# Performance work log

Measured on AMD Instinct MI355X. Metric: run time of the kernel, lower is better.

## Reference

```python
import jax, jax.numpy as jnp
import numpy as np

BS, S, D, H, HS, HSEL, L = 32, 512, 512, 8, 2, 4, 6
DK = D // H  # 64
HD = H - HS  # dynamic heads


def setup_inputs() -> dict:
    key = jax.random.key(0)
    ks = jax.random.split(key, 10)
    w = lambda k, shape: jax.random.normal(k, shape, dtype=jnp.float32) * 0.02
    return {
        'q_embed_data': jax.random.normal(ks[0], (BS, S, D), jnp.float32),
        'qa_embed_data': jax.random.normal(ks[1], (BS, S, D), jnp.float32),
        # stacked per-layer params (torch Linear convention: W[out,in], y = x@W.T+b)
        'Wq': w(ks[2], (L, D, D)), 'bq': jnp.zeros((L, D), jnp.float32),
        'Wv': w(ks[3], (L, D, D)), 'bv': jnp.zeros((L, D), jnp.float32),
        'Wg': w(ks[4], (L, HD, D)),                      # routing gate, no bias
        'Wo': w(ks[5], (L, D, D)), 'bo': jnp.zeros((L, D), jnp.float32),
        'ln1_g': jnp.ones((L, D), jnp.float32), 'ln1_b': jnp.zeros((L, D), jnp.float32),
        'W1': w(ks[6], (L, D, D)), 'b1': jnp.zeros((L, D), jnp.float32),
        'W2': w(ks[7], (L, D, D)), 'b2': jnp.zeros((L, D), jnp.float32),
        'ln2_g': jnp.ones((L, D), jnp.float32), 'ln2_b': jnp.zeros((L, D), jnp.float32),
    }


def _layer_norm(x, g, b):
    m = x.mean(-1, keepdims=True)
    v = ((x - m) ** 2).mean(-1, keepdims=True)
    return (x - m) * jax.lax.rsqrt(v + 1e-5) * g + b


def _moh_attention(xq, xv, Wq, bq, Wv, bv, Wg, Wo, bo, strict):
    bs, s, d = xq.shape
    q = xq @ Wq.T + bq            # kq_same=True: k = q projection
    v = xv @ Wv.T + bv
    qh = q.reshape(bs, s, H, DK).transpose(0, 2, 1, 3)   # [b,h,s,dk]
    vh = v.reshape(bs, s, H, DK).transpose(0, 2, 1, 3)
    scores = jnp.einsum('bhqd,bhkd->bhqk', qh, qh) / jnp.sqrt(jnp.float32(DK))
    # mask==1 -> causal incl. diag; mask==0 -> strictly causal
    allow = jnp.tril(jnp.ones((s, s), bool), k=-1 if strict else 0)
    scores = jnp.where(allow, scores, jnp.float32(-1e9))
    # pad-zero shift: first query row replaced by zeros -> uniform attention
    scores = scores.at[:, :, 0, :].set(0.0)
    # per-token top-k head routing over dynamic heads
    gates = jax.nn.softmax(q.reshape(bs * s, D) @ Wg.T, axis=-1)  # [bs*s, HD]
    _, idx = jax.lax.top_k(gates, HSEL)
    dmask = jnp.zeros_like(gates).at[jnp.arange(bs * s)[:, None], idx].set(1.0)
    dyn = (gates * dmask).reshape(bs, s, HD)
    routing = jnp.concatenate([jnp.ones((bs, s, HS), gates.dtype), dyn], -1).mean(1)  # [b,H]
    attn = jax.nn.softmax(scores, axis=-1)
    ctx = jnp.einsum('bhqk,bhkd->bhqd', attn, vh) * routing[:, :, None, None]
    out = ctx.transpose(0, 2, 1, 3).reshape(bs, s, D) @ Wo.T + bo
    f = dmask.sum(0)
    P = gates.mean(0)
    balance = jnp.sum((f / (f.sum() + 1e-5)) * (P / (P.sum() + 1e-5)))
    return out, balance


def reference(q_embed_data, qa_embed_data, Wq, bq, Wv, bv, Wg, Wo, bo,
              ln1_g, ln1_b, W1, b1, W2, b2, ln2_g, ln2_b):
    def layer(i, xq, xv, strict):
        a, bl = _moh_attention(xq, xv, Wq[i], bq[i], Wv[i], bv[i], Wg[i], Wo[i], bo[i], strict)
        x = _layer_norm(xq + a, ln1_g[i], ln1_b[i])
        ffn = jax.nn.relu(x @ W1[i].T + b1[i]) @ W2[i].T + b2[i]
        return _layer_norm(x + ffn, ln2_g[i], ln2_b[i]), bl

    y = qa_embed_data
    x = q_embed_data
    # blocks_1: self-attention on y, mask=1
    y, _ = layer(0, y, y, False)
    y, _ = layer(1, y, y, False)
    # blocks_2: alternate mask=1 self-attn / mask=0 cross-attn (values=y)
    x, _ = layer(2, x, x, False)
    x, bl = layer(3, x, y, True)
    x, _ = layer(4, x, x, False)
    x, bl = layer(5, x, y, True)
    return (x, bl)
```

## Files before the change

kernel.cpp:

```cpp
#include <hip/hip_runtime.h>
#include <cstdint>

#define BSZ 32
#define SEQ 512
#define DM  512
#define NH  8
#define DK  64
#define HS_ 2
#define HD_ 6
#define NL  6
#define MROWS (BSZ*SEQ)
#define QVLD 1024
#define SCL 0.18033688011112043f

typedef unsigned short bf16_t;
typedef __attribute__((ext_vector_type(4))) float f32x4;
typedef __attribute__((ext_vector_type(8))) short bf16x8;
typedef __attribute__((ext_vector_type(8))) unsigned short u16x8;

#define DEV static __device__ __forceinline__

DEV float bf2f(bf16_t b) {
  unsigned int u = ((unsigned int)b) << 16;
  float f; __builtin_memcpy(&f, &u, 4); return f;
}
DEV bf16_t f2b(float f) {
  unsigned int u; __builtin_memcpy(&u, &f, 4);
  unsigned int r = (u + 0x7fffu + ((u >> 16) & 1u)) >> 16;
  return (bf16_t)r;
}
DEV void unp2(unsigned int w, float& a, float& b) {
  unsigned int ua = w << 16, ub = w & 0xffff0000u;
  __builtin_memcpy(&a, &ua, 4); __builtin_memcpy(&b, &ub, 4);
}
DEV unsigned cvtpk(float lo, float hi) {
  unsigned r;
  asm("v_cvt_pk_bf16_f32 %0, %1, %2" : "=v"(r) : "v"(lo), "v"(hi));
  return r;
}

DEV void gload_lds16(const bf16_t* g, bf16_t* l) {
  __builtin_amdgcn_global_load_lds(
      (const __attribute__((address_space(1))) void*)g,
      (__attribute__((address_space(3))) void*)l, 16, 0, 0);
}

DEV bf16x8 scale_q(bf16x8 v) {
  u16x8 u;
  __builtin_memcpy(&u, &v, 16);
  unsigned w[4];
#pragma unroll
  for (int e = 0; e < 4; ++e)
    w[e] = cvtpk(bf2f(u[2 * e]) * SCL, bf2f(u[2 * e + 1]) * SCL);
  bf16x8 r;
  __builtin_memcpy(&r, w, 16);
  return r;
}

__global__ __launch_bounds__(256) void f2b2_kernel(
    const float* __restrict__ s0, const float* __restrict__ s1,
    bf16_t* __restrict__ d0, bf16_t* __restrict__ d1) {
  const float* s = blockIdx.y ? s1 : s0;
  bf16_t* d = blockIdx.y ? d1 : d0;
  const int i = blockIdx.x * 256 + threadIdx.x;
  float4 v = reinterpret_cast<const float4*>(s)[i];
  ushort4 o;
  o.x = f2b(v.x); o.y = f2b(v.y); o.z = f2b(v.z); o.w = f2b(v.w);
  reinterpret_cast<ushort4*>(d)[i] = o;
}

__global__ __launch_bounds__(256) void f2bw_kernel(
    const float* __restrict__ s0, const float* __restrict__ s1,
    const float* __restrict__ s2, const float* __restrict__ s3,
    const float* __restrict__ s4, bf16_t* __restrict__ dst) {
  const float* srcs[5] = {s0, s1, s2, s3, s4};
  const float* s = srcs[blockIdx.y];
  bf16_t* d = dst + (size_t)blockIdx.y * ((size_t)NL * DM * DM);
  const int i = blockIdx.x * 256 + threadIdx.x;
  float4 v = reinterpret_cast<const float4*>(s)[i];
  ushort4 o;
  o.x = f2b(v.x); o.y = f2b(v.y); o.z = f2b(v.z); o.w = f2b(v.w);
  reinterpret_cast<ushort4*>(d)[i] = o;
}

template <int NB, int NWG, bool RELU>
__global__ __launch_bounds__(512) void gemm8(
    const bf16_t* __restrict__ A0, const bf16_t* __restrict__ A1,
    const bf16_t* __restrict__ W0, const bf16_t* __restrict__ W1,
    const float* __restrict__ b0, const float* __restrict__ b1,
    bf16_t* __restrict__ Yb, int ldy) {
  const int K = 512;
  const int lin = blockIdx.y * NB + blockIdx.x;
  const int cpx = NWG / 8;
  const int swz = (lin & 7) * cpx + (lin >> 3);
  const int bn = swz % NB, bm = swz / NB;
  const int tid = threadIdx.x, wid = tid >> 6, lane = tid & 63;
  const int wr = wid >> 2, wc = wid & 3;
  const int lrow = lane & 15, grp = lane >> 4;
  const int l3 = lane >> 3, c3 = lane & 7;

  __shared__ __align__(16) bf16_t Lds[3][24576];

  const bool hi = (bn * 256) >= 512;
  const bf16_t* Asel = hi ? A1 : A0;
  const bf16_t* Wsel = hi ? (W1 - (size_t)512 * K) : W0;
  const float* bsel = hi ? (b1 - 512) : b0;

  f32x4 acc[4][4];
#pragma unroll
  for (int m = 0; m < 4; ++m)
#pragma unroll
    for (int n = 0; n < 4; ++n) acc[m][n] = f32x4{0.f, 0.f, 0.f, 0.f};

  const char* LB = (const char*)Lds;

  auto stage3 = [&](int kt, int buf, int half) {
#pragma unroll
    for (int cc = 0; cc < 3; ++cc) {
      const int c = wid + (half * 3 + cc) * 8;
      const int colb = ((c3 ^ l3) * 8);
      if (c < 16) {
        gload_lds16(Asel + (size_t)(bm * 128 + c * 8 + l3) * K + kt * 64 + colb,
                    &Lds[buf][c * 512]);
      } else {
        const int cb = c - 16;
        gload_lds16(Wsel + (size_t)(bn * 256 + cb * 8 + l3) * K + kt * 64 + colb,
                    &Lds[buf][8192 + cb * 512]);
      }
    }
  };
  auto rdA = [&](int buf, int rA, int ks) -> bf16x8 {
    const int off = buf * 49152 + rA * 128 + ((ks * 64 + grp * 16) ^ ((rA & 7) << 4));
    return *reinterpret_cast<const bf16x8*>(LB + off);
  };
  auto rdB = [&](int buf, int rB, int ks) -> bf16x8 {
    const int off = buf * 49152 + 16384 + rB * 128 + ((ks * 64 + grp * 16) ^ ((rB & 7) << 4));
    return *reinterpret_cast<const bf16x8*>(LB + off);
  };

  stage3(0, 0, 0); stage3(0, 0, 1);
  stage3(1, 1, 0); stage3(1, 1, 1);
  asm volatile("s_waitcnt vmcnt(6)" ::: "memory");
  __builtin_amdgcn_s_barrier();

  for (int g = 0; g < 8; ++g) {
    const int bufR = g % 3, bufW = (g + 2) % 3;
    const bool st = g < 6;
    bf16x8 bwv[4][2], afv[2][2];
#pragma unroll
    for (int n = 0; n < 4; ++n)
#pragma unroll
      for (int ks = 0; ks < 2; ++ks)
        bwv[n][ks] = rdB(bufR, wc * 64 + n * 16 + lrow, ks);
#pragma unroll
    for (int m = 0; m < 2; ++m)
#pragma unroll
      for (int ks = 0; ks < 2; ++ks)
        afv[m][ks] = rdA(bufR, wr * 64 + m * 16 + lrow, ks);
    if (st) stage3(g + 2, bufW, 0);
    __builtin_amdgcn_s_barrier();
    asm volatile("s_waitcnt lgkmcnt(0)" ::: "memory");
    __builtin_amdgcn_s_setprio(1);
#pragma unroll
    for (int ks = 0; ks < 2; ++ks)
#pragma unroll
      for (int m = 0; m < 2; ++m)
#pragma unroll
        for (int n = 0; n < 4; ++n)
          acc[m][n] = __builtin_amdgcn_mfma_f32_16x16x32_bf16(afv[m][ks], bwv[n][ks], acc[m][n], 0, 0, 0);
    __builtin_amdgcn_s_setprio(0);
    __builtin_amdgcn_s_barrier();
#pragma unroll
    for (int m = 0; m < 2; ++m)
#pragma unroll
      for (int ks = 0; ks < 2; ++ks)
        afv[m][ks] = rdA(bufR, wr * 64 + 32 + m * 16 + lrow, ks);
    if (st) stage3(g + 2, bufW, 1);
    __builtin_amdgcn_s_barrier();
    asm volatile("s_waitcnt lgkmcnt(0)" ::: "memory");
    __builtin_amdgcn_s_setprio(1);
#pragma unroll
    for (int ks = 0; ks < 2; ++ks)
#pragma unroll
      for (int m = 0; m < 2; ++m)
#pragma unroll
        for (int n = 0; n < 4; ++n)
          acc[2 + m][n] = __builtin_amdgcn_mfma_f32_16x16x32_bf16(afv[m][ks], bwv[n][ks], acc[2 + m][n], 0, 0, 0);
    __builtin_amdgcn_s_setprio(0);
    if (g < 6) {
      asm volatile("s_waitcnt vmcnt(6)" ::: "memory");
    } else if (g == 6) {
      asm volatile("s_waitcnt vmcnt(0)" ::: "memory");
    }
    __builtin_amdgcn_s_barrier();
  }

  const int r0 = bm * 128 + wr * 64 + grp * 4;
  const int c0 = bn * 256 + wc * 64 + lrow;
#pragma unroll
  for (int n = 0; n < 4; ++n) {
    const int col = c0 + n * 16;
    const float bc = bsel[col];
#pragma unroll
    for (int qm = 0; qm < 4; ++qm)
#pragma unroll
      for (int j = 0; j < 4; ++j) {
        float v = acc[qm][n][j] + bc;
        if (RELU) v = fmaxf(v, 0.f);
        Yb[(size_t)(r0 + qm * 16 + j) * ldy + col] = f2b(v);
      }
  }
}

template <int OUT>
__global__ __launch_bounds__(512) void gemm_ln(
    const bf16_t* __restrict__ A, const bf16_t* __restrict__ W,
    const float* __restrict__ bias, const bf16_t* __restrict__ Res,
    const float* __restrict__ gam, const float* __restrict__ bet,
    bf16_t* __restrict__ outb, float* __restrict__ outf) {
  const int K = 512;
  const int bm = blockIdx.x;
  const int tid = threadIdx.x, wid = tid >> 6, lane = tid & 63;
  const int lrow = lane & 15, grp = lane >> 4;
  const int l3 = lane >> 3, c3 = lane & 7;

  __shared__ __align__(16) bf16_t Lds[2][36864];
  __shared__ float red_s[64][8], red_q[64][8], stat[64][2];

  f32x4 acc[4][4];
#pragma unroll
  for (int m = 0; m < 4; ++m)
#pragma unroll
    for (int n = 0; n < 4; ++n) acc[m][n] = f32x4{0.f, 0.f, 0.f, 0.f};

  const char* LB = (const char*)Lds;

  auto stage = [&](int kt, int buf) {
#pragma unroll
    for (int k = 0; k < 9; ++k) {
      const int c = wid + k * 8;
      const int colb = (c3 ^ l3) * 8;
      if (c < 8) {
        gload_lds16(A + (size_t)(bm * 64 + c * 8 + l3) * K + kt * 64 + colb,
                    &Lds[buf][c * 512]);
      } else {
        const int cb = c - 8;
        gload_lds16(W + (size_t)(cb * 8 + l3) * K + kt * 64 + colb,
                    &Lds[buf][4096 + cb * 512]);
      }
    }
  };
  auto rdA = [&](int buf, int r, int ks) -> bf16x8 {
    const int off = buf * 73728 + r * 128 + ((ks * 64 + grp * 16) ^ ((r & 7) << 4));
    return *reinterpret_cast<const bf16x8*>(LB + off);
  };
  auto rdW = [&](int buf, int r, int ks) -> bf16x8 {
    const int off = buf * 73728 + 8192 + r * 128 + ((ks * 64 + grp * 16) ^ ((r & 7) << 4));
    return *reinterpret_cast<const bf16x8*>(LB + off);
  };

  stage(0, 0);
  __syncthreads();
  for (int g = 0; g < 8; ++g) {
    const int bufR = g & 1;
    if (g < 7) stage(g + 1, bufR ^ 1);
    bf16x8 af[4][2], wf[4][2];
#pragma unroll
    for (int m = 0; m < 4; ++m)
#pragma unroll
      for (int ks = 0; ks < 2; ++ks)
        af[m][ks] = rdA(bufR, m * 16 + lrow, ks);
#pragma unroll
    for (int n = 0; n < 4; ++n)
#pragma unroll
      for (int ks = 0; ks < 2; ++ks)
        wf[n][ks] = rdW(bufR, wid * 64 + n * 16 + lrow, ks);
    __builtin_amdgcn_s_setprio(1);
#pragma unroll
    for (int ks = 0; ks < 2; ++ks)
#pragma unroll
      for (int m = 0; m < 4; ++m)
#pragma unroll
        for (int n = 0; n < 4; ++n)
          acc[m][n] = __builtin_amdgcn_mfma_f32_16x16x32_bf16(af[m][ks], wf[n][ks], acc[m][n], 0, 0, 0);
    __builtin_amdgcn_s_setprio(0);
    __syncthreads();
  }

  const int cbase = wid * 64;
  float bias_n[4], gam_n[4], bet_n[4];
#pragma unroll
  for (int n = 0; n < 4; ++n) {
    bias_n[n] = bias[cbase + n * 16 + lrow];
    gam_n[n]  = gam[cbase + n * 16 + lrow];
    bet_n[n]  = bet[cbase + n * 16 + lrow];
  }
  const size_t rowg0 = (size_t)bm * 64;
  float ps[4][4], pq[4][4];
#pragma unroll
  for (int m = 0; m < 4; ++m)
#pragma unroll
    for (int j = 0; j < 4; ++j) {
      const int r = m * 16 + grp * 4 + j;
      float s = 0.f, q = 0.f;
#pragma unroll
      for (int n = 0; n < 4; ++n) {
        float z = acc[m][n][j] + bias_n[n] +
                  bf2f(Res[(rowg0 + r) * DM + cbase + n * 16 + lrow]);
        acc[m][n][j] = z;
        s += z; q += z * z;
      }
      ps[m][j] = s; pq[m][j] = q;
    }
#pragma unroll
  for (int m = 0; m < 4; ++m)
#pragma unroll
    for (int j = 0; j < 4; ++j)
#pragma unroll
      for (int off = 1; off <= 8; off <<= 1) {
        ps[m][j] += __shfl_xor(ps[m][j], off);
        pq[m][j] += __shfl_xor(pq[m][j], off);
      }
  if (lrow == 0) {
#pragma unroll
    for (int m = 0; m < 4; ++m)
#pragma unroll
      for (int j = 0; j < 4; ++j) {
        const int r = m * 16 + grp * 4 + j;
        red_s[r][wid] = ps[m][j];
        red_q[r][wid] = pq[m][j];
      }
  }
  __syncthreads();
  if (tid < 64) {
    float s = 0.f, q = 0.f;
#pragma unroll
    for (int w = 0; w < 8; ++w) { s += red_s[tid][w]; q += red_q[tid][w]; }
    const float mean = s * (1.f / 512.f);
    const float var = q * (1.f / 512.f) - mean * mean;
    stat[tid][0] = mean;
    stat[tid][1] = rsqrtf(var + 1e-5f);
  }
  __syncthreads();
#pragma unroll
  for (int m = 0; m < 4; ++m)
#pragma unroll
    for (int j = 0; j < 4; ++j) {
      const int r = m * 16 + grp * 4 + j;
      const float mean = stat[r][0], rstd = stat[r][1];
#pragma unroll
      for (int n = 0; n < 4; ++n) {
        const float o = (acc[m][n][j] - mean) * rstd * gam_n[n] + bet_n[n];
        const size_t off = (rowg0 + r) * DM + cbase + n * 16 + lrow;
        if (OUT == 0) outb[off] = f2b(o);
        else outf[off] = o;
      }
    }
}

__global__ __launch_bounds__(256) void gates_kernel(
    const bf16_t* __restrict__ qv, const float* __restrict__ Wg,
    float* __restrict__ rdyn, float* __restrict__ fP) {
  __shared__ float wg_s[HD_ * DM];
  __shared__ float blk[4][18];
  const int tid = threadIdx.x, wid = tid >> 6, lane = tid & 63;
  for (int i = tid; i < HD_ * DM / 4; i += 256)
    reinterpret_cast<float4*>(wg_s)[i] = reinterpret_cast<const float4*>(Wg)[i];
  __syncthreads();
  const int bb = blockIdx.x >> 4;
  const int t0 = (blockIdx.x & 15) * 32 + wid * 8;
  float fs[6] = {0, 0, 0, 0, 0, 0}, ps[6] = {0, 0, 0, 0, 0, 0}, rs[6] = {0, 0, 0, 0, 0, 0};
  for (int it = 0; it < 8; ++it) {
    const int tok = bb * SEQ + t0 + it;
    uint4 u = reinterpret_cast<const uint4*>(qv + (size_t)tok * QVLD)[lane];
    float x[8];
    unp2(u.x, x[0], x[1]); unp2(u.y, x[2], x[3]);
    unp2(u.z, x[4], x[5]); unp2(u.w, x[6], x[7]);
    float g[6];
#pragma unroll
    for (int j = 0; j < 6; ++j) {
      float p = 0.f;
#pragma unroll
      for (int e = 0; e < 8; ++e) p = fmaf(x[e], wg_s[j * DM + lane * 8 + e], p);
#pragma unroll
      for (int off = 32; off; off >>= 1) p += __shfl_xor(p, off);
      g[j] = p;
    }
    float mx = g[0];
#pragma unroll
    for (int j = 1; j < 6; ++j) mx = fmaxf(mx, g[j]);
    float se = 0.f;
#pragma unroll
    for (int j = 0; j < 6; ++j) { g[j] = __expf(g[j] - mx); se += g[j]; }
    float inv = 1.f / se;
#pragma unroll
    for (int j = 0; j < 6; ++j) g[j] *= inv;
    int d1 = 0;
#pragma unroll
    for (int j = 1; j < 6; ++j)
      if (g[j] < g[d1] || (g[j] == g[d1] && j > d1)) d1 = j;
    int d2 = (d1 == 0) ? 1 : 0;
#pragma unroll
    for (int j = 0; j < 6; ++j) {
      if (j == d1) continue;
      if (g[j] < g[d2] || (g[j] == g[d2] && j > d2)) d2 = j;
    }
#pragma unroll
    for (int j = 0; j < 6; ++j) {
      const bool drop = (j == d1) || (j == d2);
      fs[j] += drop ? 0.f : 1.f;
      ps[j] += g[j];
      rs[j] += drop ? 0.f : g[j];
    }
  }
  if (lane == 0) {
#pragma unroll
    for (int j = 0; j < 6; ++j) {
      blk[wid][j] = fs[j]; blk[wid][6 + j] = ps[j]; blk[wid][12 + j] = rs[j];
    }
  }
  __syncthreads();
  if (tid < 18) {
    float s = blk[0][tid] + blk[1][tid] + blk[2][tid] + blk[3][tid];
    if (tid < 12) atomicAdd(&fP[tid], s);
    else atomicAdd(&rdyn[bb * 6 + (tid - 12)], s * (1.f / 512.f));
  }
}

__global__ __launch_bounds__(256, 2) void fattn_kernel(
    const bf16_t* __restrict__ qv, const float* __restrict__ rdyn,
    bf16_t* __restrict__ ctx, int strict) {
  const int bh = blockIdx.x, qt = blockIdx.y;
  const int b = bh >> 3, h = bh & 7;
  const int tid = threadIdx.x, wid = tid >> 6, lane = tid & 63;
  const int c0 = lane & 15, grp = lane >> 4;
  const int l3 = lane >> 3, c3 = lane & 7;
  const int kidx = lane & 31, dhalf = lane >> 5;

  __shared__ __align__(16) bf16_t Ks[64 * 64];
  __shared__ __align__(16) bf16_t Vt[64 * 72];
  __shared__ __align__(16) bf16_t Ps[4][32 * 64];
  __shared__ float csum[64];

  const bf16_t* qp = qv;
  const bf16_t* vp = qv + 512;
  const float factor = (h < HS_) ? 1.f : rdyn[b * 6 + (h - HS_)];

  const int qbase = qt * 128 + wid * 32;

  bf16x8 qf[2][2];
#pragma unroll
  for (int nt = 0; nt < 2; ++nt)
#pragma unroll
    for (int ks = 0; ks < 2; ++ks)
      qf[nt][ks] = scale_q(*reinterpret_cast<const bf16x8*>(
          qp + ((size_t)(b * SEQ + qbase + nt * 16 + c0)) * QVLD + h * DK + ks * 32 + grp * 8));

  f32x4 acc[2][4];
#pragma unroll
  for (int m = 0; m < 2; ++m)
#pragma unroll
    for (int d = 0; d < 4; ++d) acc[m][d] = f32x4{0.f, 0.f, 0.f, 0.f};
  float mreg[2] = {-3e38f, -3e38f};
  float lreg[2] = {0.f, 0.f};
  float cs[8] = {0, 0, 0, 0, 0, 0, 0, 0};

  const int lastk = (qbase + 31 - strict) >> 6;
  const int ktmax = 2 * qt + 1;

  for (int kt = 0; kt <= ktmax; ++kt) {
#pragma unroll
    for (int i = 0; i < 2; ++i) {
      int row = i * 32 + wid * 8 + l3;
      int blk = c3 ^ l3;
      gload_lds16(qp + ((size_t)(b * SEQ + kt * 64 + row)) * QVLD + h * DK + blk * 8,
                  Ks + (i * 32 + wid * 8) * 64);
    }
#pragma unroll
    for (int j = 0; j < 2; ++j) {
      const int d0 = (wid * 2 + j) * 8 + dhalf * 4;
      const bf16_t* src = vp + ((size_t)(b * SEQ + kt * 64 + 2 * kidx)) * QVLD + h * DK + d0;
      ushort4 lo = *reinterpret_cast<const ushort4*>(src);
      ushort4 hv = *reinterpret_cast<const ushort4*>(src + QVLD);
      *reinterpret_cast<unsigned*>(&Vt[(d0 + 0) * 72 + 2 * kidx]) = (unsigned)lo.x | ((unsigned)hv.x << 16);
      *reinterpret_cast<unsigned*>(&Vt[(d0 + 1) * 72 + 2 * kidx]) = (unsigned)lo.y | ((unsigned)hv.y << 16);
      *reinterpret_cast<unsigned*>(&Vt[(d0 + 2) * 72 + 2 * kidx]) = (unsigned)lo.z | ((unsigned)hv.z << 16);
      *reinterpret_cast<unsigned*>(&Vt[(d0 + 3) * 72 + 2 * kidx]) = (unsigned)lo.w | ((unsigned)hv.w << 16);
      if (qt == 3) {
        cs[j * 4 + 0] += bf2f(lo.x) + bf2f(hv.x);
        cs[j * 4 + 1] += bf2f(lo.y) + bf2f(hv.y);
        cs[j * 4 + 2] += bf2f(lo.z) + bf2f(hv.z);
        cs[j * 4 + 3] += bf2f(lo.w) + bf2f(hv.w);
      }
    }
    __syncthreads();

    if (kt <= lastk) {
      const char* KsB = (const char*)Ks;
      bf16x8 kf[4][2];
#pragma unroll
      for (int mt = 0; mt < 4; ++mt)
#pragma unroll
        for (int ks = 0; ks < 2; ++ks)
          kf[mt][ks] = *reinterpret_cast<const bf16x8*>(
              KsB + (mt * 16 + c0) * 128 + 16 * ((4 * ks + grp) ^ (c0 & 7)));
      f32x4 s[4][2];
#pragma unroll
      for (int mt = 0; mt < 4; ++mt)
#pragma unroll
        for (int nt = 0; nt < 2; ++nt) s[mt][nt] = f32x4{0.f, 0.f, 0.f, 0.f};
      __builtin_amdgcn_s_setprio(1);
#pragma unroll
      for (int mt = 0; mt < 4; ++mt)
#pragma unroll
        for (int nt = 0; nt < 2; ++nt)
#pragma unroll
          for (int ks = 0; ks < 2; ++ks)
            s[mt][nt] = __builtin_amdgcn_mfma_f32_16x16x32_bf16(
                kf[mt][ks], qf[nt][ks], s[mt][nt], 0, 0, 0);
      __builtin_amdgcn_s_setprio(0);

      const bool masked = (kt == lastk);
      if (masked) {
#pragma unroll
        for (int nt = 0; nt < 2; ++nt) {
          const int q = qbase + nt * 16 + c0;
#pragma unroll
          for (int mt = 0; mt < 4; ++mt)
#pragma unroll
            for (int j = 0; j < 4; ++j) {
              int k = kt * 64 + mt * 16 + grp * 4 + j;
              if (k + strict > q) s[mt][nt][j] = -1e30f;
            }
        }
      }
      float mx[2];
#pragma unroll
      for (int nt = 0; nt < 2; ++nt) {
        float a = fmaxf(s[0][nt][0], s[0][nt][1]);
        a = fmaxf(fmaxf(a, s[0][nt][2]), s[0][nt][3]);
        float bm_ = fmaxf(s[1][nt][0], s[1][nt][1]);
        bm_ = fmaxf(fmaxf(bm_, s[1][nt][2]), s[1][nt][3]);
        float c = fmaxf(s[2][nt][0], s[2][nt][1]);
        c = fmaxf(fmaxf(c, s[2][nt][2]), s[2][nt][3]);
        float d = fmaxf(s[3][nt][0], s[3][nt][1]);
        d = fmaxf(fmaxf(d, s[3][nt][2]), s[3][nt][3]);
        float m_ = fmaxf(fmaxf(a, bm_), fmaxf(c, d));
        m_ = fmaxf(m_, __shfl_xor(m_, 16));
        m_ = fmaxf(m_, __shfl_xor(m_, 32));
        mx[nt] = m_;
      }
      const bool defer = __all((mx[0] - mreg[0] <= 8.f) && (mx[1] - mreg[1] <= 8.f));
      float sc[2];
#pragma unroll
      for (int nt = 0; nt < 2; ++nt) {
        const float mnew = defer ? mreg[nt] : fmaxf(mreg[nt], mx[nt]);
        float ts = 0.f;
#pragma unroll
        for (int mt = 0; mt < 4; ++mt)
#pragma unroll
          for (int j = 0; j < 4; ++j) {
            float pp = exp2f(s[mt][nt][j] - mnew);
            s[mt][nt][j] = pp; ts += pp;
          }
        ts += __shfl_xor(ts, 16);
        ts += __shfl_xor(ts, 32);
        if (defer) {
          lreg[nt] += ts;
        } else {
          sc[nt] = exp2f(mreg[nt] - mnew);
          lreg[nt] = lreg[nt] * sc[nt] + ts;
          mreg[nt] = mnew;
        }
      }
      char* PsB = (char*)(&Ps[wid][0]);
#pragma unroll
      for (int nt = 0; nt < 2; ++nt)
#pragma unroll
        for (int mt = 0; mt < 4; ++mt) {
          uint2 w;
          w.x = cvtpk(s[mt][nt][0], s[mt][nt][1]);
          w.y = cvtpk(s[mt][nt][2], s[mt][nt][3]);
          int row = nt * 16 + c0;
          int off = (row * 128 + mt * 32 + grp * 8) ^ ((c0 & 7) << 4);
          *reinterpret_cast<uint2*>(PsB + off) = w;
        }
      if (!defer) {
#pragma unroll
        for (int mtq = 0; mtq < 2; ++mtq) {
          f32x4 sv;
#pragma unroll
          for (int j = 0; j < 4; ++j) sv[j] = __shfl(sc[mtq], grp * 4 + j);
#pragma unroll
          for (int dt = 0; dt < 4; ++dt) acc[mtq][dt] *= sv;
        }
      }
      bf16x8 pf[2][2], vf2[4][2];
#pragma unroll
      for (int mtq = 0; mtq < 2; ++mtq)
#pragma unroll
        for (int ks = 0; ks < 2; ++ks)
          pf[mtq][ks] = *reinterpret_cast<const bf16x8*>(
              PsB + (mtq * 16 + c0) * 128 + 16 * ((4 * ks + grp) ^ (c0 & 7)));
#pragma unroll
      for (int dt = 0; dt < 4; ++dt)
#pragma unroll
        for (int ks = 0; ks < 2; ++ks)
          vf2[dt][ks] = *reinterpret_cast<const bf16x8*>(
              (const char*)Vt + (dt * 16 + c0) * 144 + ks * 64 + grp * 16);
      __builtin_amdgcn_s_setprio(1);
#pragma unroll
      for (int mtq = 0; mtq < 2; ++mtq)
#pragma unroll
        for (int dt = 0; dt < 4; ++dt)
#pragma unroll
          for (int ks = 0; ks < 2; ++ks)
            acc[mtq][dt] = __builtin_amdgcn_mfma_f32_16x16x32_bf16(
                pf[mtq][ks], vf2[dt][ks], acc[mtq][dt], 0, 0, 0);
      __builtin_amdgcn_s_setprio(0);
    }
    __syncthreads();
  }

  if (qt == 3) {
#pragma unroll
    for (int e = 0; e < 8; ++e)
#pragma unroll
      for (int off = 1; off <= 16; off <<= 1) cs[e] += __shfl_xor(cs[e], off);
    if ((lane & 31) == 0) {
#pragma unroll
      for (int e = 0; e < 8; ++e)
        csum[(wid * 2 + (e >> 2)) * 8 + dhalf * 4 + (e & 3)] = cs[e];
    }
    __syncthreads();
    if (tid < 64)
      ctx[((size_t)(b * SEQ)) * DM + h * DK + tid] = f2b(csum[tid] * (1.f / 512.f) * factor);
  }

#pragma unroll
  for (int mtq = 0; mtq < 2; ++mtq) {
    const float inv = factor / lreg[mtq];
    f32x4 iv;
#pragma unroll
    for (int j = 0; j < 4; ++j) iv[j] = __shfl(inv, grp * 4 + j);
#pragma unroll
    for (int j = 0; j < 4; ++j) {
      const int q = qbase + mtq * 16 + grp * 4 + j;
      if (q == 0) continue;
#pragma unroll
      for (int dt = 0; dt < 4; ++dt)
        ctx[((size_t)(b * SEQ + q)) * DM + h * DK + dt * 16 + c0] =
            f2b(acc[mtq][dt][j] * iv[j]);
    }
  }
}

__global__ void balance_kernel(const float* __restrict__ fP, float* __restrict__ out) {
  if (threadIdx.x == 0 && blockIdx.x == 0) {
    float fs = 0.f, pssum = 0.f, P[6];
    for (int j = 0; j < 6; ++j) {
      fs += fP[j];
      P[j] = fP[6 + j] * (1.f / (float)MROWS);
      pssum += P[j];
    }
    float bal = 0.f;
    for (int j = 0; j < 6; ++j)
      bal += (fP[j] / (fs + 1e-5f)) * (P[j] / (pssum + 1e-5f));
    out[0] = bal;
  }
}

extern "C" void kernel_launch(void* const* d_in, const int* in_sizes, int n_in,
                              void* d_out, int out_size, void* d_ws, size_t ws_size,
                              hipStream_t stream) {
  (void)in_sizes; (void)n_in; (void)out_size; (void)ws_size;
  const float* q_embed  = (const float*)d_in[0];
  const float* qa_embed = (const float*)d_in[1];
  const float* Wq  = (const float*)d_in[2];
  const float* bq  = (const float*)d_in[3];
  const float* Wv  = (const float*)d_in[4];
  const float* bv  = (const float*)d_in[5];
  const float* Wg  = (const float*)d_in[6];
  const float* Wo  = (const float*)d_in[7];
  const float* bo  = (const float*)d_in[8];
  const float* ln1g = (const float*)d_in[9];
  const float* ln1b = (const float*)d_in[10];
  const float* W1  = (const float*)d_in[11];
  const float* b1  = (const float*)d_in[12];
  const float* W2  = (const float*)d_in[13];
  const float* b2  = (const float*)d_in[14];
  const float* ln2g = (const float*)d_in[15];
  const float* ln2b = (const float*)d_in[16];

  char* p = (char*)d_ws;
  auto alloc = [&](size_t bytes) -> char* {
    char* r = p; p += (bytes + 255) & ~(size_t)255; return r;
  };
  const size_t WDE = (size_t)NL * DM * DM;
  const size_t AE  = (size_t)MROWS * DM;
  bf16_t* wall_b = (bf16_t*)alloc(5 * WDE * 2);
  bf16_t* wq_b = wall_b;
  bf16_t* wv_b = wall_b + WDE;
  bf16_t* wo_b = wall_b + 2 * WDE;
  bf16_t* w1_b = wall_b + 3 * WDE;
  bf16_t* w2_b = wall_b + 4 * WDE;
  bf16_t* y_b   = (bf16_t*)alloc(AE * 2);
  bf16_t* x_b   = (bf16_t*)alloc(AE * 2);
  bf16_t* qv_b  = (bf16_t*)alloc((size_t)MROWS * QVLD * 2);
  bf16_t* ctx_b = (bf16_t*)alloc(AE * 2);
  bf16_t* x1_b  = (bf16_t*)alloc(AE * 2);
  bf16_t* ffn1_b = (bf16_t*)alloc(AE * 2);
  float* stats = (float*)alloc(NL * (12 + BSZ * 6) * 4);
  float* fPbase = stats;
  float* rdynbase = stats + NL * 12;

  hipMemsetAsync(stats, 0, NL * (12 + BSZ * 6) * 4, stream);

  f2bw_kernel<<<dim3((unsigned)(WDE / 4 / 256), 5), 256, 0, stream>>>(
      Wq, Wv, Wo, W1, W2, wall_b);
  f2b2_kernel<<<dim3((unsigned)(AE / 4 / 256), 2), 256, 0, stream>>>(
      qa_embed, q_embed, y_b, x_b);

  const size_t DD = (size_t)DM * DM;
  dim3 gqv(4, 128), gn5(2, 128), gfa(256, 4), gln(256);
  float* outx = (float*)d_out;

  auto layer = [&](int i, bf16_t* resb, const bf16_t* xvb, int strict, bool last) {
    float* fP = fPbase + i * 12;
    float* rdyn = rdynbase + i * (BSZ * 6);
    gemm8<4, 512, false><<<gqv, 512, 0, stream>>>(
        resb, xvb, wq_b + i * DD, wv_b + i * DD, bq + i * DM, bv + i * DM, qv_b, QVLD);
    gates_kernel<<<MROWS / 32, 256, 0, stream>>>(qv_b, Wg + (size_t)i * HD_ * DM, rdyn, fP);
    fattn_kernel<<<gfa, 256, 0, stream>>>(qv_b, rdyn, ctx_b, strict);
    gemm_ln<0><<<gln, 512, 0, stream>>>(
        ctx_b, wo_b + i * DD, bo + i * DM, resb, ln1g + i * DM, ln1b + i * DM,
        x1_b, nullptr);
    gemm8<2, 256, true><<<gn5, 512, 0, stream>>>(
        x1_b, x1_b, w1_b + i * DD, w1_b + i * DD, b1 + i * DM, b1 + i * DM, ffn1_b, DM);
    if (last)
      gemm_ln<1><<<gln, 512, 0, stream>>>(
          ffn1_b, w2_b + i * DD, b2 + i * DM, x1_b, ln2g + i * DM, ln2b + i * DM,
          nullptr, outx);
    else
      gemm_ln<0><<<gln, 512, 0, stream>>>(
          ffn1_b, w2_b + i * DD, b2 + i * DM, x1_b, ln2g + i * DM, ln2b + i * DM,
          resb, nullptr);
  };

  layer(0, y_b, y_b, 0, false);
  layer(1, y_b, y_b, 0, false);
  layer(2, x_b, x_b, 0, false);
  layer(3, x_b, y_b, 1, false);
  layer(4, x_b, x_b, 0, false);
  layer(5, x_b, y_b, 1, true);
  balance_kernel<<<1, 64, 0, stream>>>(fPbase + 5 * 12, outx + (size_t)MROWS * DM);
}
```

Baseline: 887.7 us.

## Restructure gemm_ln into 4-wave, triple-buffered K=32 pipeline with wider per-wave tiles

The fused GEMM+LayerNorm kernel now runs 256 threads (4 waves) instead of 8. Each wave computes 128 output columns, and K is stepped in 32-wide slices through a 3-deep LDS ring buffer. Explicit vmcnt waits and raw barriers replace __syncthreads, so loads can stay two stages ahead of the MFMAs. The cost is fewer waves per block and more accumulator registers, which may lower occupancy. The new unswizzled LDS layout may also cause bank conflicts.

```diff
diff --git a/kernel.cpp b/kernel.cpp
--- a/kernel.cpp
+++ b/kernel.cpp
@@ -213,7 +213,7 @@
 }
 
 template <int OUT>
-__global__ __launch_bounds__(512) void gemm_ln(
+__global__ __launch_bounds__(256) void gemm_ln(
     const bf16_t* __restrict__ A, const bf16_t* __restrict__ W,
     const float* __restrict__ bias, const bf16_t* __restrict__ Res,
     const float* __restrict__ gam, const float* __restrict__ bet,
@@ -222,75 +222,74 @@
   const int bm = blockIdx.x;
   const int tid = threadIdx.x, wid = tid >> 6, lane = tid & 63;
   const int lrow = lane & 15, grp = lane >> 4;
-  const int l3 = lane >> 3, c3 = lane & 7;
-
-  __shared__ __align__(16) bf16_t Lds[2][36864];
-  __shared__ float red_s[64][8], red_q[64][8], stat[64][2];
-
-  f32x4 acc[4][4];
+  const int prow = lane >> 2, pcol = (lane & 3) * 8;
+
+  __shared__ __align__(16) bf16_t Lds[3][18432];
+  __shared__ float red_s[64][4], red_q[64][4], stat[64][2];
+
+  f32x4 acc[4][8];
 #pragma unroll
   for (int m = 0; m < 4; ++m)
 #pragma unroll
-    for (int n = 0; n < 4; ++n) acc[m][n] = f32x4{0.f, 0.f, 0.f, 0.f};
+    for (int n = 0; n < 8; ++n) acc[m][n] = f32x4{0.f, 0.f, 0.f, 0.f};
 
   const char* LB = (const char*)Lds;
 
   auto stage = [&](int kt, int buf) {
 #pragma unroll
     for (int k = 0; k < 9; ++k) {
-      const int c = wid + k * 8;
-      const int colb = (c3 ^ l3) * 8;
-      if (c < 8) {
-        gload_lds16(A + (size_t)(bm * 64 + c * 8 + l3) * K + kt * 64 + colb,
+      const int c = wid * 9 + k;
+      if (c < 4) {
+        gload_lds16(A + (size_t)(bm * 64 + c * 16 + prow) * K + kt * 32 + pcol,
                     &Lds[buf][c * 512]);
       } else {
-        const int cb = c - 8;
-        gload_lds16(W + (size_t)(cb * 8 + l3) * K + kt * 64 + colb,
-                    &Lds[buf][4096 + cb * 512]);
+        const int w = c - 4;
+        gload_lds16(W + (size_t)(w * 16 + prow) * K + kt * 32 + pcol,
+                    &Lds[buf][2048 + w * 512]);
       }
     }
   };
-  auto rdA = [&](int buf, int r, int ks) -> bf16x8 {
-    const int off = buf * 73728 + r * 128 + ((ks * 64 + grp * 16) ^ ((r & 7) << 4));
+  auto rdA = [&](int buf, int r) -> bf16x8 {
+    const int off = buf * 36864 + ((r >> 4) * 512 + (r & 15) * 32 + grp * 8) * 2;
     return *reinterpret_cast<const bf16x8*>(LB + off);
   };
-  auto rdW = [&](int buf, int r, int ks) -> bf16x8 {
-    const int off = buf * 73728 + 8192 + r * 128 + ((ks * 64 + grp * 16) ^ ((r & 7) << 4));
+  auto rdW = [&](int buf, int r) -> bf16x8 {
+    const int off = buf * 36864 + (2048 + (r >> 4) * 512 + (r & 15) * 32 + grp * 8) * 2;
     return *reinterpret_cast<const bf16x8*>(LB + off);
   };
 
-  stage(0, 0);
-  __syncthreads();
-  for (int g = 0; g < 8; ++g) {
-    const int bufR = g & 1;
-    if (g < 7) stage(g + 1, bufR ^ 1);
-    bf16x8 af[4][2], wf[4][2];
+  stage(0, 0); stage(1, 1);
+  asm volatile("s_waitcnt vmcnt(9)" ::: "memory");
+  __builtin_amdgcn_s_barrier();
+
+  for (int g = 0; g < 16; ++g) {
+    const int bufR = g % 3;
+    if (g < 14) stage(g + 2, (g + 2) % 3);
+    bf16x8 af[4], wf[8];
+#pragma unroll
+    for (int m = 0; m < 4; ++m) af[m] = rdA(bufR, m * 16 + lrow);
+#pragma unroll
+    for (int n = 0; n < 8; ++n) wf[n] = rdW(bufR, wid * 128 + n * 16 + lrow);
+    asm volatile("s_waitcnt lgkmcnt(0)" ::: "memory");
+    __builtin_amdgcn_s_setprio(1);
 #pragma unroll
     for (int m = 0; m < 4; ++m)
 #pragma unroll
-      for (int ks = 0; ks < 2; ++ks)
-        af[m][ks] = rdA(bufR, m * 16 + lrow, ks);
-#pragma unroll
-    for (int n = 0; n < 4; ++n)
-#pragma unroll
-      for (int ks = 0; ks < 2; ++ks)
-        wf[n][ks] = rdW(bufR, wid * 64 + n * 16 + lrow, ks);
-    __builtin_amdgcn_s_setprio(1);
-#pragma unroll
-    for (int ks = 0; ks < 2; ++ks)
-#pragma unroll
-      for (int m = 0; m < 4; ++m)
-#pragma unroll
-        for (int n = 0; n < 4; ++n)
-          acc[m][n] = __builtin_amdgcn_mfma_f32_16x16x32_bf16(af[m][ks], wf[n][ks], acc[m][n], 0, 0, 0);
+      for (int n = 0; n < 8; ++n)
+        acc[m][n] = __builtin_amdgcn_mfma_f32_16x16x32_bf16(af[m], wf[n], acc[m][n], 0, 0, 0);
     __builtin_amdgcn_s_setprio(0);
-    __syncthreads();
-  }
-
-  const int cbase = wid * 64;
-  float bias_n[4], gam_n[4], bet_n[4];
-#pragma unroll
-  for (int n = 0; n < 4; ++n) {
+    if (g < 14) {
+      asm volatile("s_waitcnt vmcnt(9)" ::: "memory");
+    } else if (g == 14) {
+      asm volatile("s_waitcnt vmcnt(0)" ::: "memory");
+    }
+    __builtin_amdgcn_s_barrier();
+  }
+
+  const int cbase = wid * 128;
+  float bias_n[8], gam_n[8], bet_n[8];
+#pragma unroll
+  for (int n = 0; n < 8; ++n) {
     bias_n[n] = bias[cbase + n * 16 + lrow];
     gam_n[n]  = gam[cbase + n * 16 + lrow];
     bet_n[n]  = bet[cbase + n * 16 + lrow];
@@ -304,7 +303,7 @@
       const int r = m * 16 + grp * 4 + j;
       float s = 0.f, q = 0.f;
 #pragma unroll
-      for (int n = 0; n < 4; ++n) {
+      for (int n = 0; n < 8; ++n) {
         float z = acc[m][n][j] + bias_n[n] +
                   bf2f(Res[(rowg0 + r) * DM + cbase + n * 16 + lrow]);
         acc[m][n][j] = z;
@@ -335,7 +334,7 @@
   if (tid < 64) {
     float s = 0.f, q = 0.f;
 #pragma unroll
-    for (int w = 0; w < 8; ++w) { s += red_s[tid][w]; q += red_q[tid][w]; }
+    for (int w = 0; w < 4; ++w) { s += red_s[tid][w]; q += red_q[tid][w]; }
     const float mean = s * (1.f / 512.f);
     const float var = q * (1.f / 512.f) - mean * mean;
     stat[tid][0] = mean;
@@ -349,7 +348,7 @@
       const int r = m * 16 + grp * 4 + j;
       const float mean = stat[r][0], rstd = stat[r][1];
 #pragma unroll
-      for (int n = 0; n < 4; ++n) {
+      for (int n = 0; n < 8; ++n) {
         const float o = (acc[m][n][j] - mean) * rstd * gam_n[n] + bet_n[n];
         const size_t off = (rowg0 + r) * DM + cbase + n * 16 + lrow;
         if (OUT == 0) outb[off] = f2b(o);
@@ -732,17 +731,17 @@
         resb, xvb, wq_b + i * DD, wv_b + i * DD, bq + i * DM, bv + i * DM, qv_b, QVLD);
     gates_kernel<<<MROWS / 32, 256, 0, stream>>>(qv_b, Wg + (size_t)i * HD_ * DM, rdyn, fP);
     fattn_kernel<<<gfa, 256, 0, stream>>>(qv_b, rdyn, ctx_b, strict);
-    gemm_ln<0><<<gln, 512, 0, stream>>>(
+    gemm_ln<0><<<gln, 256, 0, stream>>>(
         ctx_b, wo_b + i * DD, bo + i * DM, resb, ln1g + i * DM, ln1b + i * DM,
         x1_b, nullptr);
     gemm8<2, 256, true><<<gn5, 512, 0, stream>>>(
         x1_b, x1_b, w1_b + i * DD, w1_b + i * DD, b1 + i * DM, b1 + i * DM, ffn1_b, DM);
     if (last)
-      gemm_ln<1><<<gln, 512, 0, stream>>>(
+      gemm_ln<1><<<gln, 256, 0, stream>>>(
           ffn1_b, w2_b + i * DD, b2 + i * DM, x1_b, ln2g + i * DM, ln2b + i * DM,
           nullptr, outx);
     else
-      gemm_ln<0><<<gln, 512, 0, stream>>>(
+      gemm_ln<0><<<gln, 256, 0, stream>>>(
           ffn1_b, w2_b + i * DD, b2 + i * DM, x1_b, ln2g + i * DM, ln2b + i * DM,
           resb, nullptr);
   };
```

After: 974.5 us. 1.1x slower.
